# Performance work log

Hardware: AMD Instinct MI355X
Metric: run time of the kernel (lower is better)

## Reference

```python
import jax, jax.numpy as jnp
import numpy as np

B, S, D, H = 4, 2048, 256, 8
DH = D // H
DFF = 4 * D
EPS = 1e-5


def _layernorm(x, w, b):
    mu = jnp.mean(x, axis=-1, keepdims=True)
    var = jnp.mean((x - mu) ** 2, axis=-1, keepdims=True)
    return (x - mu) * jax.lax.rsqrt(var + EPS) * w + b


def setup_inputs() -> dict:
    key = jax.random.key(0)
    ks = jax.random.split(key, 16)
    s = 0.02
    return {
        "x": jax.random.normal(ks[0], (B, S, D), jnp.float32),
        "in_proj_w": jax.random.normal(ks[1], (3 * D, D), jnp.float32) * s,
        "in_proj_b": jax.random.normal(ks[2], (3 * D,), jnp.float32) * s,
        "out_w": jax.random.normal(ks[3], (D, D), jnp.float32) * s,
        "out_b": jax.random.normal(ks[4], (D,), jnp.float32) * s,
        "ln1_w": jnp.ones((D,), jnp.float32),
        "ln1_b": jnp.zeros((D,), jnp.float32),
        "ln2_w": jnp.ones((D,), jnp.float32),
        "ln2_b": jnp.zeros((D,), jnp.float32),
        "ff1_w": jax.random.normal(ks[5], (DFF, D), jnp.float32) * s,
        "ff1_b": jax.random.normal(ks[6], (DFF,), jnp.float32) * s,
        "ff2_w": jax.random.normal(ks[7], (D, DFF), jnp.float32) * s,
        "ff2_b": jax.random.normal(ks[8], (D,), jnp.float32) * s,
        "slopes": jax.random.normal(ks[9], (H, 1, 1), jnp.float32),
    }


def reference(x, in_proj_w, in_proj_b, out_w, out_b, ln1_w, ln1_b, ln2_w, ln2_b,
              ff1_w, ff1_b, ff2_w, ff2_b, slopes):
    # learned ALiBi-style relative bias: (H, S, S)
    pos = jnp.arange(S, dtype=jnp.float32)
    rel = jnp.abs(pos[None, :] - pos[:, None])          # (S, S)
    bias = -jnp.abs(slopes) * rel[None, :, :]           # (H, S, S)

    xn = _layernorm(x, ln1_w, ln1_b)
    qkv = jnp.einsum('bsd,ed->bse', xn, in_proj_w) + in_proj_b
    q, k, v = jnp.split(qkv, 3, axis=-1)
    # (B, H, S, DH)
    q = q.reshape(B, S, H, DH).transpose(0, 2, 1, 3)
    k = k.reshape(B, S, H, DH).transpose(0, 2, 1, 3)
    v = v.reshape(B, S, H, DH).transpose(0, 2, 1, 3)

    scores = jnp.einsum('bhqd,bhkd->bhqk', q, k) / jnp.sqrt(jnp.float32(DH))
    scores = scores + bias[None, :, :, :]
    attn = jax.nn.softmax(scores, axis=-1)
    ctx = jnp.einsum('bhqk,bhkd->bhqd', attn, v)
    ctx = ctx.transpose(0, 2, 1, 3).reshape(B, S, D)
    attn_out = jnp.einsum('bsd,ed->bse', ctx, out_w) + out_b

    x = x + attn_out
    xn2 = _layernorm(x, ln2_w, ln2_b)
    h = jnp.einsum('bsd,fd->bsf', xn2, ff1_w) + ff1_b
    h = jax.nn.gelu(h, approximate=False)
    ff_out = jnp.einsum('bsf,df->bsd', h, ff2_w) + ff2_b
    return x + ff_out
```

## Files before the change

### kernel.cpp

```cpp
#include <hip/hip_runtime.h>
#include <hip/hip_bf16.h>
#include <math.h>

#define S_LEN 2048
#define D_MODEL 256
#define N_HEADS 8
#define HEAD_DIM 32
#define D_FF 1024
#define ROWS_TOTAL 8192

typedef __attribute__((ext_vector_type(8))) short short8;
typedef __attribute__((ext_vector_type(4))) float f32x4;

__device__ inline ushort f2bf(float f) {
    unsigned u = __builtin_bit_cast(unsigned, f);
    unsigned r = (u + 0x7fffu + ((u >> 16) & 1u)) >> 16;
    return (ushort)r;
}

__device__ inline float bf2f(ushort u) {
    return __builtin_bit_cast(float, ((unsigned)u) << 16);
}

__device__ inline unsigned cvtpk(float a, float b) {
    unsigned r;
    asm("v_cvt_pk_bf16_f32 %0, %1, %2" : "=v"(r) : "v"(a), "v"(b));
    return r;
}

__global__ __launch_bounds__(256) void prep_kernel(
    const float* __restrict__ w0, const float* __restrict__ w1,
    const float* __restrict__ w2, const float* __restrict__ w3,
    ushort* __restrict__ o0, ushort* __restrict__ o1,
    ushort* __restrict__ o2, ushort* __restrict__ o3,
    const float* __restrict__ x, const float* __restrict__ lnw,
    const float* __restrict__ lnb, ushort* __restrict__ xnb) {
    int blk = blockIdx.x;
    if (blk < 768) {
        int i = blk * 256 + threadIdx.x;
        const float* src;
        ushort* dst;
        int off;
        if (i < 49152)       { src = w0; dst = o0; off = i; }
        else if (i < 65536)  { src = w1; dst = o1; off = i - 49152; }
        else if (i < 131072) { src = w2; dst = o2; off = i - 65536; }
        else                 { src = w3; dst = o3; off = i - 131072; }
        float4 v = ((const float4*)src)[off];
        ushort4 u = {f2bf(v.x), f2bf(v.y), f2bf(v.z), f2bf(v.w)};
        ((ushort4*)dst)[off] = u;
    } else {
        int wid = threadIdx.x >> 6, lane = threadIdx.x & 63;
        int row = (blk - 768) * 4 + wid;
        float4 v = ((const float4*)(x + (size_t)row * D_MODEL))[lane];
        float4 wv = ((const float4*)lnw)[lane];
        float4 bv = ((const float4*)lnb)[lane];
        float s = v.x + v.y + v.z + v.w;
        float s2 = v.x * v.x + v.y * v.y + v.z * v.z + v.w * v.w;
        #pragma unroll
        for (int off = 1; off < 64; off <<= 1) {
            s  += __shfl_xor(s, off);
            s2 += __shfl_xor(s2, off);
        }
        float mu = s * (1.0f / D_MODEL);
        float var = s2 * (1.0f / D_MODEL) - mu * mu;
        float rstd = rsqrtf(var + 1e-5f);
        ushort4 o = {f2bf((v.x - mu) * rstd * wv.x + bv.x), f2bf((v.y - mu) * rstd * wv.y + bv.y),
                     f2bf((v.z - mu) * rstd * wv.z + bv.z), f2bf((v.w - mu) * rstd * wv.w + bv.w)};
        ((ushort4*)(xnb + (size_t)row * D_MODEL))[lane] = o;
    }
}

template <int EPI, int BM, int BN>
__global__ __launch_bounds__(256) void gemm_mfma(
    const ushort* __restrict__ A,
    const ushort* __restrict__ W,
    const float* __restrict__ bias,
    const void* __restrict__ resid,
    float* __restrict__ outf,
    ushort* __restrict__ outh,
    ushort* __restrict__ qout, ushort* __restrict__ kout, ushort* __restrict__ vout,
    int M, int N, int K) {
    constexpr int MR = BM / 32;
    constexpr int NR = BN / 32;
    __shared__ ushort As[BM * 64];
    __shared__ ushort Bs[BN * 64];
    const int tid = threadIdx.x;
    const int lane = tid & 63, wid = tid >> 6;
    const int l15 = lane & 15, hi = lane >> 4;
    const int wr = wid >> 1, wc = wid & 1;
    const int row0 = blockIdx.x * BM, col0 = blockIdx.y * BN;

    f32x4 acc[MR][NR];
    #pragma unroll
    for (int m = 0; m < MR; m++)
        #pragma unroll
        for (int n = 0; n < NR; n++) acc[m][n] = (f32x4){0.f, 0.f, 0.f, 0.f};

    short8 sa[MR], sb[NR];
    #pragma unroll
    for (int t = 0; t < MR; t++) {
        int c = tid + t * 256;
        sa[t] = *(const short8*)(A + (size_t)(row0 + (c >> 3)) * K + (c & 7) * 8);
    }
    #pragma unroll
    for (int t = 0; t < NR; t++) {
        int c = tid + t * 256;
        sb[t] = *(const short8*)(W + (size_t)(col0 + (c >> 3)) * K + (c & 7) * 8);
    }

    for (int k0 = 0; k0 < K; k0 += 64) {
        __syncthreads();
        #pragma unroll
        for (int t = 0; t < MR; t++) {
            int c = tid + t * 256;
            int r = c >> 3, cb = (c & 7) * 16;
            *(short8*)((char*)As + r * 128 + (cb ^ ((r & 7) << 4))) = sa[t];
        }
        #pragma unroll
        for (int t = 0; t < NR; t++) {
            int c = tid + t * 256;
            int r = c >> 3, cb = (c & 7) * 16;
            *(short8*)((char*)Bs + r * 128 + (cb ^ ((r & 7) << 4))) = sb[t];
        }
        __syncthreads();
        if (k0 + 64 < K) {
            #pragma unroll
            for (int t = 0; t < MR; t++) {
                int c = tid + t * 256;
                sa[t] = *(const short8*)(A + (size_t)(row0 + (c >> 3)) * K + k0 + 64 + (c & 7) * 8);
            }
            #pragma unroll
            for (int t = 0; t < NR; t++) {
                int c = tid + t * 256;
                sb[t] = *(const short8*)(W + (size_t)(col0 + (c >> 3)) * K + k0 + 64 + (c & 7) * 8);
            }
        }
        #pragma unroll
        for (int ks = 0; ks < 2; ks++) {
            short8 af[MR], bfr[NR];
            #pragma unroll
            for (int m = 0; m < MR; m++) {
                int r = wr * (BM / 2) + m * 16 + l15;
                af[m] = *(const short8*)((char*)As + r * 128 + ((ks * 64 + hi * 16) ^ ((r & 7) << 4)));
            }
            #pragma unroll
            for (int n = 0; n < NR; n++) {
                int r = wc * (BN / 2) + n * 16 + l15;
                bfr[n] = *(const short8*)((char*)Bs + r * 128 + ((ks * 64 + hi * 16) ^ ((r & 7) << 4)));
            }
            #pragma unroll
            for (int m = 0; m < MR; m++)
                #pragma unroll
                for (int n = 0; n < NR; n++)
                    acc[m][n] = __builtin_amdgcn_mfma_f32_16x16x32_bf16(af[m], bfr[n], acc[m][n], 0, 0, 0);
        }
    }

    #pragma unroll
    for (int m = 0; m < MR; m++) {
        #pragma unroll
        for (int n = 0; n < NR; n++) {
            #pragma unroll
            for (int r = 0; r < 4; r++) {
                int row = row0 + wr * (BM / 2) + m * 16 + hi * 4 + r;
                int col = col0 + wc * (BN / 2) + n * 16 + l15;
                float val = acc[m][n][r] + bias[col];
                if (EPI == 0) {
                    int part = col >> 8;
                    int d_o = col & 255;
                    int hh = d_o >> 5, dh = d_o & 31;
                    int bbb = row >> 11, s = row & 2047;
                    size_t bhi = (size_t)bbb * N_HEADS + hh;
                    if (part == 0) {
                        qout[(bhi * S_LEN + s) * HEAD_DIM + dh] = f2bf(val * 0.2550347137f);
                    } else {
                        int tt = s >> 6, k = s & 63;
                        size_t tb = (bhi * 32 + tt) * 2048;
                        if (part == 1)
                            kout[tb + (dh >> 3) * 512 + k * 8 + (dh & 7)] = f2bf(val);
                        else
                            vout[tb + ((size_t)((k >> 5) * 4 + ((k >> 3) & 3))) * 256 + dh * 8 + (k & 7)] = f2bf(val);
                    }
                } else if (EPI == 2) {
                    float g = 0.5f * val * (1.f + erff(val * 0.70710678118654752f));
                    outh[(size_t)row * N + col] = f2bf(g);
                } else {
                    float rv = bf2f(((const ushort*)resid)[(size_t)row * N + col]);
                    outf[(size_t)row * N + col] = rv + val;
                }
            }
        }
    }
}

__global__ __launch_bounds__(256) void gemm_opln(
    const ushort* __restrict__ A,
    const ushort* __restrict__ W,
    const float* __restrict__ bias,
    const float* __restrict__ residf,
    const float* __restrict__ lnw, const float* __restrict__ lnb,
    ushort* __restrict__ xnb, ushort* __restrict__ x1b) {
    __shared__ ushort As[16 * 64];
    __shared__ ushort Bs[256 * 64];
    __shared__ float red[4][16][2];
    const int tid = threadIdx.x;
    const int lane = tid & 63, wc = tid >> 6;
    const int l15 = lane & 15, hi = lane >> 4;
    const int row0 = blockIdx.x * 16;

    f32x4 acc[4];
    #pragma unroll
    for (int n = 0; n < 4; n++) acc[n] = (f32x4){0.f, 0.f, 0.f, 0.f};

    short8 sa, sb[8];
    if (tid < 128)
        sa = *(const short8*)(A + (size_t)(row0 + (tid >> 3)) * 256 + (tid & 7) * 8);
    #pragma unroll
    for (int t = 0; t < 8; t++) {
        int c = tid + t * 256;
        sb[t] = *(const short8*)(W + (size_t)(c >> 3) * 256 + (c & 7) * 8);
    }

    for (int k0 = 0; k0 < 256; k0 += 64) {
        __syncthreads();
        if (tid < 128) {
            int r = tid >> 3, cb = (tid & 7) * 16;
            *(short8*)((char*)As + r * 128 + (cb ^ ((r & 7) << 4))) = sa;
        }
        #pragma unroll
        for (int t = 0; t < 8; t++) {
            int c = tid + t * 256;
            int r = c >> 3, cb = (c & 7) * 16;
            *(short8*)((char*)Bs + r * 128 + (cb ^ ((r & 7) << 4))) = sb[t];
        }
        __syncthreads();
        if (k0 + 64 < 256) {
            if (tid < 128)
                sa = *(const short8*)(A + (size_t)(row0 + (tid >> 3)) * 256 + k0 + 64 + (tid & 7) * 8);
            #pragma unroll
            for (int t = 0; t < 8; t++) {
                int c = tid + t * 256;
                sb[t] = *(const short8*)(W + (size_t)(c >> 3) * 256 + k0 + 64 + (c & 7) * 8);
            }
        }
        #pragma unroll
        for (int ks = 0; ks < 2; ks++) {
            short8 af, bfr[4];
            {
                int r = l15;
                af = *(const short8*)((char*)As + r * 128 + ((ks * 64 + hi * 16) ^ ((r & 7) << 4)));
            }
            #pragma unroll
            for (int n = 0; n < 4; n++) {
                int r = wc * 64 + n * 16 + l15;
                bfr[n] = *(const short8*)((char*)Bs + r * 128 + ((ks * 64 + hi * 16) ^ ((r & 7) << 4)));
            }
            #pragma unroll
            for (int n = 0; n < 4; n++)
                acc[n] = __builtin_amdgcn_mfma_f32_16x16x32_bf16(af, bfr[n], acc[n], 0, 0, 0);
        }
    }

    float x1v[4][4];
    float s1[4], s2[4];
    #pragma unroll
    for (int r = 0; r < 4; r++) { s1[r] = 0.f; s2[r] = 0.f; }
    #pragma unroll
    for (int n = 0; n < 4; n++) {
        #pragma unroll
        for (int r = 0; r < 4; r++) {
            int row = row0 + hi * 4 + r;
            int col = wc * 64 + n * 16 + l15;
            float v = acc[n][r] + bias[col] + residf[(size_t)row * 256 + col];
            x1v[n][r] = v;
            s1[r] += v;
            s2[r] += v * v;
        }
    }
    #pragma unroll
    for (int r = 0; r < 4; r++) {
        #pragma unroll
        for (int off = 1; off < 16; off <<= 1) {
            s1[r] += __shfl_xor(s1[r], off);
            s2[r] += __shfl_xor(s2[r], off);
        }
    }
    if (l15 == 0) {
        #pragma unroll
        for (int r = 0; r < 4; r++) {
            red[wc][hi * 4 + r][0] = s1[r];
            red[wc][hi * 4 + r][1] = s2[r];
        }
    }
    __syncthreads();
    #pragma unroll
    for (int r = 0; r < 4; r++) {
        int rl = hi * 4 + r;
        float a1 = red[0][rl][0] + red[1][rl][0] + red[2][rl][0] + red[3][rl][0];
        float a2 = red[0][rl][1] + red[1][rl][1] + red[2][rl][1] + red[3][rl][1];
        float mu = a1 * (1.0f / 256.f);
        float var = a2 * (1.0f / 256.f) - mu * mu;
        float rstd = rsqrtf(var + 1e-5f);
        size_t row = row0 + rl;
        #pragma unroll
        for (int n = 0; n < 4; n++) {
            int col = wc * 64 + n * 16 + l15;
            float v = x1v[n][r];
            xnb[row * 256 + col] = f2bf((v - mu) * rstd * lnw[col] + lnb[col]);
            x1b[row * 256 + col] = f2bf(v);
        }
    }
}

__global__ __launch_bounds__(256) void attn_mfma(
    const ushort* __restrict__ qb, const ushort* __restrict__ kb,
    const ushort* __restrict__ vt, const float* __restrict__ slopes,
    ushort* __restrict__ ctxout) {
    __shared__ ushort plds[4][1024];
    const int tid = threadIdx.x;
    const int wid = tid >> 6, lane = tid & 63;
    const int l15 = lane & 15, hi = lane >> 4;
    const int bh = blockIdx.y, h = bh & (N_HEADS - 1), bb = bh >> 3;
    const int qt = blockIdx.x * 4 + wid;
    const int qbase = qt * 16;
    const float slope = fabsf(slopes[h]) * 1.4426950408889634f;

    const int wl = (int)fminf(2048.f, 32.f / fmaxf(slope, 1e-6f));
    const int tlo = max(0, (qbase - wl) >> 6);
    const int thi = min(31, (qbase + 15 + wl) >> 6);

    const ushort* Kg = kb + (size_t)bh * 32 * 2048;
    const ushort* Vg = vt + (size_t)bh * 32 * 2048;

    short8 qf = *(const short8*)(qb + ((size_t)bh * S_LEN + qbase + l15) * HEAD_DIM + hi * 8);

    f32x4 ctxa[2];
    ctxa[0] = (f32x4){0.f, 0.f, 0.f, 0.f};
    ctxa[1] = (f32x4){0.f, 0.f, 0.f, 0.f};
    float lsum = 0.f;

    char* pw = (char*)&plds[wid][0];
    const int bpi = lane & 0x30;
    const int wr_off = ((hi >> 1) << 8) + (l15 << 4) + ((hi & 1) << 3);
    const int rd0 = (hi << 8) + (l15 << 4);

    const float qoff = (float)(qbase + l15 - 4 * hi);

    short8 kfc[4], vfc[2][2];
    {
        const ushort* Kt = Kg + (size_t)tlo * 2048;
        const ushort* Vt = Vg + (size_t)tlo * 2048;
        #pragma unroll
        for (int c = 0; c < 4; c++)
            kfc[c] = *(const short8*)(Kt + (hi * 64 + 16 * c + l15) * 8);
        #pragma unroll
        for (int f = 0; f < 2; f++)
            #pragma unroll
            for (int dt = 0; dt < 2; dt++)
                vfc[f][dt] = *(const short8*)(Vt + ((f * 4 + hi) * 32 + dt * 16 + l15) * 8);
    }

    for (int t = tlo; t <= thi; ++t) {
        short8 kfn[4], vfn[2][2];
        if (t < thi) {
            const ushort* Kt = Kg + (size_t)(t + 1) * 2048;
            const ushort* Vt = Vg + (size_t)(t + 1) * 2048;
            #pragma unroll
            for (int c = 0; c < 4; c++)
                kfn[c] = *(const short8*)(Kt + (hi * 64 + 16 * c + l15) * 8);
            #pragma unroll
            for (int f = 0; f < 2; f++)
                #pragma unroll
                for (int dt = 0; dt < 2; dt++)
                    vfn[f][dt] = *(const short8*)(Vt + ((f * 4 + hi) * 32 + dt * 16 + l15) * 8);
        }

        const f32x4 z = {0.f, 0.f, 0.f, 0.f};
        f32x4 s[4];
        __builtin_amdgcn_s_setprio(1);
        #pragma unroll
        for (int c = 0; c < 4; c++)
            s[c] = __builtin_amdgcn_mfma_f32_16x16x32_bf16(kfc[c], qf, z, 0, 0, 0);
        __builtin_amdgcn_s_setprio(0);

        float dkt = qoff - (float)(64 * t);
        #pragma unroll
        for (int c = 0; c < 4; c++) {
            float d0 = dkt - (float)(16 * c);
            #pragma unroll
            for (int r = 0; r < 4; r++)
                s[c][r] = exp2f(fmaf(-slope, fabsf(d0 - (float)r), s[c][r]));
        }
        f32x4 t01 = s[0] + s[1], t23 = s[2] + s[3];
        f32x4 tt = t01 + t23;
        float tsum = (tt[0] + tt[1]) + (tt[2] + tt[3]);
        tsum += __shfl_xor(tsum, 16);
        tsum += __shfl_xor(tsum, 32);
        lsum += tsum;

        #pragma unroll
        for (int c = 0; c < 4; c++) {
            unsigned lo  = cvtpk(s[c][0], s[c][1]);
            unsigned hi2 = cvtpk(s[c][2], s[c][3]);
            *(unsigned long long*)(pw + (c << 9) + wr_off) =
                ((unsigned long long)hi2 << 32) | (unsigned long long)lo;
        }
        asm volatile("s_waitcnt lgkmcnt(0)" ::: "memory");
        short8 pa0 = *(const short8*)(pw + rd0);
        short8 pa1 = *(const short8*)(pw + 1024 + rd0);
        __builtin_amdgcn_s_setprio(1);
        #pragma unroll
        for (int dt = 0; dt < 2; dt++) {
            ctxa[dt] = __builtin_amdgcn_mfma_f32_16x16x32_bf16(pa0, vfc[0][dt], ctxa[dt], 0, 0, 0);
            ctxa[dt] = __builtin_amdgcn_mfma_f32_16x16x32_bf16(pa1, vfc[1][dt], ctxa[dt], 0, 0, 0);
        }
        __builtin_amdgcn_s_setprio(0);

        #pragma unroll
        for (int c = 0; c < 4; c++) kfc[c] = kfn[c];
        #pragma unroll
        for (int f = 0; f < 2; f++)
            #pragma unroll
            for (int dt = 0; dt < 2; dt++) vfc[f][dt] = vfn[f][dt];
    }
    float inv = 1.f / lsum;
    int invi = __builtin_bit_cast(int, inv);
    #pragma unroll
    for (int r = 0; r < 4; r++) {
        float ir = __builtin_bit_cast(float, __builtin_amdgcn_ds_bpermute(bpi + 4 * r, invi));
        size_t row = (size_t)bb * S_LEN + qbase + 4 * hi + r;
        #pragma unroll
        for (int dt = 0; dt < 2; dt++)
            ctxout[row * D_MODEL + h * HEAD_DIM + dt * 16 + l15] = f2bf(ctxa[dt][r] * ir);
    }
}

extern "C" void kernel_launch(void* const* d_in, const int* in_sizes, int n_in,
                              void* d_out, int out_size, void* d_ws, size_t ws_size,
                              hipStream_t stream) {
    const float* x      = (const float*)d_in[0];
    const float* in_w   = (const float*)d_in[1];
    const float* in_b   = (const float*)d_in[2];
    const float* outw   = (const float*)d_in[3];
    const float* outb   = (const float*)d_in[4];
    const float* ln1w   = (const float*)d_in[5];
    const float* ln1b   = (const float*)d_in[6];
    const float* ln2w   = (const float*)d_in[7];
    const float* ln2b   = (const float*)d_in[8];
    const float* ff1w   = (const float*)d_in[9];
    const float* ff1b   = (const float*)d_in[10];
    const float* ff2w   = (const float*)d_in[11];
    const float* ff2b   = (const float*)d_in[12];
    const float* slopes = (const float*)d_in[13];
    float* out = (float*)d_out;

    const size_t SZ = (size_t)ROWS_TOTAL * D_MODEL;
    ushort* xnb   = (ushort*)d_ws;
    ushort* ctxb  = xnb + SZ;
    ushort* qb16  = ctxb + SZ;
    ushort* kb16  = qb16 + SZ;
    ushort* vt16  = kb16 + SZ;
    ushort* hbb   = vt16 + SZ;
    ushort* wqkvb = hbb + 4 * SZ;
    ushort* woutb = wqkvb + 768 * 256;
    ushort* wff1b = woutb + 256 * 256;
    ushort* wff2b = wff1b + 1024 * 256;
    ushort* x1b   = wff2b + 256 * 1024;

    prep_kernel<<<768 + ROWS_TOTAL / 4, 256, 0, stream>>>(
        in_w, outw, ff1w, ff2w, wqkvb, woutb, wff1b, wff2b, x, ln1w, ln1b, xnb);
    gemm_mfma<0, 64, 128><<<dim3(ROWS_TOTAL / 64, 768 / 128), 256, 0, stream>>>(
        xnb, wqkvb, in_b, nullptr, nullptr, nullptr, qb16, kb16, vt16, ROWS_TOTAL, 768, D_MODEL);
    attn_mfma<<<dim3(32, 32), 256, 0, stream>>>(qb16, kb16, vt16, slopes, ctxb);
    gemm_opln<<<ROWS_TOTAL / 16, 256, 0, stream>>>(
        ctxb, woutb, outb, x, ln2w, ln2b, xnb, x1b);
    gemm_mfma<2, 64, 128><<<dim3(ROWS_TOTAL / 64, D_FF / 128), 256, 0, stream>>>(
        xnb, wff1b, ff1b, nullptr, nullptr, hbb, nullptr, nullptr, nullptr, ROWS_TOTAL, D_FF, D_MODEL);
    gemm_mfma<5, 64, 64><<<dim3(ROWS_TOTAL / 64, D_MODEL / 64), 256, 0, stream>>>(
        hbb, wff2b, ff2b, x1b, out, nullptr, nullptr, nullptr, nullptr, ROWS_TOTAL, D_MODEL, D_FF);
}
```

Baseline: 74.85 us.

## Add dedicated FF2 GEMM kernel with BK=128 swizzled LDS and register prefetch

```diff
diff --git a/kernel.cpp b/kernel.cpp
--- a/kernel.cpp
+++ b/kernel.cpp
@@ -57,9 +57,9 @@
         float s = v.x + v.y + v.z + v.w;
         float s2 = v.x * v.x + v.y * v.y + v.z * v.z + v.w * v.w;
         #pragma unroll
-        for (int off = 1; off < 64; off <<= 1) {
-            s  += __shfl_xor(s, off);
-            s2 += __shfl_xor(s2, off);
+        for (int off2 = 1; off2 < 64; off2 <<= 1) {
+            s  += __shfl_xor(s, off2);
+            s2 += __shfl_xor(s2, off2);
         }
         float mu = s * (1.0f / D_MODEL);
         float var = s2 * (1.0f / D_MODEL) - mu * mu;
@@ -184,10 +184,92 @@
                 } else if (EPI == 2) {
                     float g = 0.5f * val * (1.f + erff(val * 0.70710678118654752f));
                     outh[(size_t)row * N + col] = f2bf(g);
-                } else {
-                    float rv = bf2f(((const ushort*)resid)[(size_t)row * N + col]);
-                    outf[(size_t)row * N + col] = rv + val;
                 }
+            }
+        }
+    }
+}
+
+__global__ __launch_bounds__(256) void gemm_ff2k(
+    const ushort* __restrict__ A,
+    const ushort* __restrict__ W,
+    const float* __restrict__ bias,
+    const ushort* __restrict__ resid,
+    float* __restrict__ outf) {
+    __shared__ ushort As[64 * 128];
+    __shared__ ushort Bs[64 * 128];
+    const int tid = threadIdx.x;
+    const int lane = tid & 63, wid = tid >> 6;
+    const int l15 = lane & 15, hi = lane >> 4;
+    const int wr = wid >> 1, wc = wid & 1;
+    const int row0 = blockIdx.x * 64, col0 = blockIdx.y * 64;
+
+    f32x4 acc[2][2];
+    #pragma unroll
+    for (int m = 0; m < 2; m++)
+        #pragma unroll
+        for (int n = 0; n < 2; n++) acc[m][n] = (f32x4){0.f, 0.f, 0.f, 0.f};
+
+    short8 sa[4], sb[4];
+    #pragma unroll
+    for (int t = 0; t < 4; t++) {
+        int c = tid + t * 256;
+        int r = c >> 4, e = (c & 15) * 8;
+        sa[t] = *(const short8*)(A + (size_t)(row0 + r) * 1024 + e);
+        sb[t] = *(const short8*)(W + (size_t)(col0 + r) * 1024 + e);
+    }
+
+    for (int k0 = 0; k0 < 1024; k0 += 128) {
+        __syncthreads();
+        #pragma unroll
+        for (int t = 0; t < 4; t++) {
+            int c = tid + t * 256;
+            int r = c >> 4, cb = (c & 15) * 16;
+            int sw = cb ^ ((r & 7) << 4);
+            *(short8*)((char*)As + r * 256 + sw) = sa[t];
+            *(short8*)((char*)Bs + r * 256 + sw) = sb[t];
+        }
+        __syncthreads();
+        if (k0 + 128 < 1024) {
+            #pragma unroll
+            for (int t = 0; t < 4; t++) {
+                int c = tid + t * 256;
+                int r = c >> 4, e = (c & 15) * 8;
+                sa[t] = *(const short8*)(A + (size_t)(row0 + r) * 1024 + k0 + 128 + e);
+                sb[t] = *(const short8*)(W + (size_t)(col0 + r) * 1024 + k0 + 128 + e);
+            }
+        }
+        #pragma unroll
+        for (int ks = 0; ks < 4; ks++) {
+            short8 af[2], bfr[2];
+            #pragma unroll
+            for (int m = 0; m < 2; m++) {
+                int r = wr * 32 + m * 16 + l15;
+                af[m] = *(const short8*)((char*)As + r * 256 + ((ks * 64 + hi * 16) ^ ((r & 7) << 4)));
+            }
+            #pragma unroll
+            for (int n = 0; n < 2; n++) {
+                int r = wc * 32 + n * 16 + l15;
+                bfr[n] = *(const short8*)((char*)Bs + r * 256 + ((ks * 64 + hi * 16) ^ ((r & 7) << 4)));
+            }
+            #pragma unroll
+            for (int m = 0; m < 2; m++)
+                #pragma unroll
+                for (int n = 0; n < 2; n++)
+                    acc[m][n] = __builtin_amdgcn_mfma_f32_16x16x32_bf16(af[m], bfr[n], acc[m][n], 0, 0, 0);
+        }
+    }
+
+    #pragma unroll
+    for (int m = 0; m < 2; m++) {
+        #pragma unroll
+        for (int n = 0; n < 2; n++) {
+            #pragma unroll
+            for (int r = 0; r < 4; r++) {
+                int row = row0 + wr * 32 + m * 16 + hi * 4 + r;
+                int col = col0 + wc * 32 + n * 16 + l15;
+                float rv = bf2f(resid[(size_t)row * 256 + col]);
+                outf[(size_t)row * 256 + col] = acc[m][n][r] + bias[col] + rv;
             }
         }
     }
@@ -476,6 +558,6 @@
         ctxb, woutb, outb, x, ln2w, ln2b, xnb, x1b);
     gemm_mfma<2, 64, 128><<<dim3(ROWS_TOTAL / 64, D_FF / 128), 256, 0, stream>>>(
         xnb, wff1b, ff1b, nullptr, nullptr, hbb, nullptr, nullptr, nullptr, ROWS_TOTAL, D_FF, D_MODEL);
-    gemm_mfma<5, 64, 64><<<dim3(ROWS_TOTAL / 64, D_MODEL / 64), 256, 0, stream>>>(
-        hbb, wff2b, ff2b, x1b, out, nullptr, nullptr, nullptr, nullptr, ROWS_TOTAL, D_MODEL, D_FF);
-}
+    gemm_ff2k<<<dim3(ROWS_TOTAL / 64, D_MODEL / 64), 256, 0, stream>>>(
+        hbb, wff2b, ff2b, x1b, out);
+}
```

Result: no change. 74.04 us (-1.1%).
